# Performance work log

Hardware: AMD Instinct MI355X
Metric: run time of the kernel (lower is better)

The kernel has to match this reference:

```python
import jax, jax.numpy as jnp
import numpy as np

# RT-DETR matcher hyperparameters (from config)
ALPHA, GAMMA = 0.25, 2.0
C_CLASS, C_BBOX, C_GIOU = 2.0, 5.0, 2.0
B, Q, C, T = 32, 300, 80, 100  # batch, queries, classes, targets-per-image


def _center_to_corners(b):
    cx, cy, w, h = jnp.split(b, 4, axis=-1)
    return jnp.concatenate([cx - 0.5 * w, cy - 0.5 * h, cx + 0.5 * w, cy + 0.5 * h], axis=-1)


def _generalized_box_iou(boxes1, boxes2):
    # boxes1 [N,4], boxes2 [M,4] in corner format -> [N,M] GIoU
    area1 = (boxes1[:, 2] - boxes1[:, 0]) * (boxes1[:, 3] - boxes1[:, 1])
    area2 = (boxes2[:, 2] - boxes2[:, 0]) * (boxes2[:, 3] - boxes2[:, 1])
    lt = jnp.maximum(boxes1[:, None, :2], boxes2[None, :, :2])
    rb = jnp.minimum(boxes1[:, None, 2:], boxes2[None, :, 2:])
    wh = jnp.clip(rb - lt, 0.0)
    inter = wh[..., 0] * wh[..., 1]
    union = area1[:, None] + area2[None, :] - inter
    iou = inter / union
    lt_e = jnp.minimum(boxes1[:, None, :2], boxes2[None, :, :2])
    rb_e = jnp.maximum(boxes1[:, None, 2:], boxes2[None, :, 2:])
    wh_e = jnp.clip(rb_e - lt_e, 0.0)
    enclose = wh_e[..., 0] * wh_e[..., 1]
    return iou - (enclose - union) / enclose


def setup_inputs() -> dict:
    key = jax.random.key(0)
    k1, k2, k3, k4 = jax.random.split(key, 4)
    logits = jax.random.normal(k1, (B, Q, C), dtype=jnp.float32)
    pred_boxes = jax.random.uniform(k2, (B, Q, 4), dtype=jnp.float32)
    target_labels = jax.random.randint(k3, (B * T,), 0, C)
    target_boxes = jax.random.uniform(k4, (B * T, 4), dtype=jnp.float32)
    return {"logits": logits, "pred_boxes": pred_boxes,
            "target_labels": target_labels, "target_boxes": target_boxes}


def reference(logits, pred_boxes, target_labels, target_boxes):
    batch_size, num_queries, num_classes = logits.shape
    out_bbox = pred_boxes.reshape(-1, 4)                      # [B*Q, 4]
    # focal-style class cost (use_focal_loss=True)
    out_prob = jax.nn.sigmoid(logits.reshape(-1, num_classes))  # [B*Q, C]
    out_prob = out_prob[:, target_labels]                       # [B*Q, B*T]
    neg_cost = (1 - ALPHA) * out_prob ** GAMMA * -jnp.log(1 - out_prob + 1e-8)
    pos_cost = ALPHA * (1 - out_prob) ** GAMMA * -jnp.log(out_prob + 1e-8)
    class_cost = pos_cost - neg_cost
    # pairwise L1 cost on cxcywh boxes
    bbox_cost = jnp.sum(jnp.abs(out_bbox[:, None, :] - target_boxes[None, :, :]), axis=-1)
    # pairwise GIoU cost on corner boxes
    giou_cost = -_generalized_box_iou(_center_to_corners(out_bbox), _center_to_corners(target_boxes))
    cost_matrix = C_BBOX * bbox_cost + C_CLASS * class_cost + C_GIOU * giou_cost
    return cost_matrix.reshape(batch_size, num_queries, -1)    # [B, Q, B*T]
```

## Files before the change

### kernel.cpp

```cpp
#include <hip/hip_runtime.h>


constexpr int BB = 32, QQ = 300, CN = 80, TT = 100;
constexpr int NQ = BB * QQ;
constexpr int NT = BB * TT;
constexpr int JG = NT / 4;
constexpr int RCHUNK = 32;
constexpr int STRIPES = (JG + 255) / 256;
constexpr int CCN = RCHUNK * CN;

typedef float vfloat4 __attribute__((ext_vector_type(4)));

__global__ __launch_bounds__(256, 4) void fused_kernel(
    const float*  __restrict__ logits,
    const float4* __restrict__ pred_boxes,
    const int*    __restrict__ labels,
    const float4* __restrict__ target_boxes,
    float4*       __restrict__ out)
{
  const int tid  = threadIdx.x;
  const int jg   = blockIdx.x * 256 + tid;
  const int row0 = blockIdx.y * RCHUNK;

  __shared__ float  s_cc[CCN];
  __shared__ float4 s_pred[RCHUNK];

  const float* lgbase = logits + (size_t)row0 * CN;
#pragma unroll
  for (int i = 0; i < CCN / 256; ++i) {
    const int e = i * 256 + tid;
    float x = lgbase[e];
    float p = 1.0f / (1.0f + __expf(-x));
    float omp = 1.0f - p;
    float neg = 0.75f * p * p * (-__logf(omp + 1e-8f));
    float pos = 0.25f * omp * omp * (-__logf(p + 1e-8f));
    s_cc[e] = 2.0f * (pos - neg) + 2.0f;
  }
  if (tid < RCHUNK) s_pred[tid] = pred_boxes[row0 + tid];
  __syncthreads();
  if (jg >= JG) return;

  float tcx[4], tcy[4], tw[4], th[4];
  float tx0[4], ty0[4], tx1[4], ty1[4], ta[4];
  const float* ccbase[4];
#pragma unroll
  for (int k = 0; k < 4; ++k) {
    float4 t = target_boxes[jg * 4 + k];
    tcx[k] = t.x; tcy[k] = t.y; tw[k] = t.z; th[k] = t.w;
    tx0[k] = t.x - 0.5f * t.z;  ty0[k] = t.y - 0.5f * t.w;
    tx1[k] = t.x + 0.5f * t.z;  ty1[k] = t.y + 0.5f * t.w;
    ta[k]  = t.z * t.w;
    ccbase[k] = s_cc + labels[jg * 4 + k];
  }

  vfloat4* outp = reinterpret_cast<vfloat4*>(out + (size_t)row0 * JG + jg);

  for (int rb = 0; rb < RCHUNK; rb += 4) {
#pragma unroll
    for (int ri = 0; ri < 4; ++ri) {
      const int r = rb + ri;
      float4 p = s_pred[r];
      float px0 = p.x - 0.5f * p.z, py0 = p.y - 0.5f * p.w;
      float px1 = p.x + 0.5f * p.z, py1 = p.y + 0.5f * p.w;
      float pa  = p.z * p.w;

      float res[4];
#pragma unroll
      for (int k = 0; k < 4; ++k) {
        float l1 = fabsf(p.x - tcx[k]) + fabsf(p.y - tcy[k]) +
                   fabsf(p.z - tw[k])  + fabsf(p.w - th[k]);
        float ltx = fmaxf(px0, tx0[k]), lty = fmaxf(py0, ty0[k]);
        float rbx = fminf(px1, tx1[k]), rby = fminf(py1, ty1[k]);
        float iw = fmaxf(rbx - ltx, 0.0f), ih = fmaxf(rby - lty, 0.0f);
        float inter = iw * ih;
        float uni = pa + ta[k] - inter;
        float ex0 = fminf(px0, tx0[k]), ey0 = fminf(py0, ty0[k]);
        float ex1 = fmaxf(px1, tx1[k]), ey1 = fmaxf(py1, ty1[k]);
        float enc = (ex1 - ex0) * (ey1 - ey0);
        float iou = inter * __builtin_amdgcn_rcpf(uni);
        float une = uni   * __builtin_amdgcn_rcpf(enc);
        float cls = ccbase[k][r * CN];
        float acc = fmaf(5.0f, l1, cls);
        acc       = fmaf(-2.0f, iou, acc);
        res[k]    = fmaf(-2.0f, une, acc);
      }
      vfloat4 v = { res[0], res[1], res[2], res[3] };
      __builtin_nontemporal_store(v, &outp[(size_t)r * JG]);
    }
  }
}

extern "C" void kernel_launch(void* const* d_in, const int* in_sizes, int n_in,
                              void* d_out, int out_size, void* d_ws, size_t ws_size,
                              hipStream_t stream) {
  const float*  logits = (const float*)d_in[0];
  const float4* pred   = (const float4*)d_in[1];
  const int*    labels = (const int*)d_in[2];
  const float4* tboxes = (const float4*)d_in[3];
  float4* out = (float4*)d_out;

  dim3 grid(STRIPES, NQ / RCHUNK);
  fused_kernel<<<grid, 256, 0, stream>>>(logits, pred, labels, tboxes, out);
}
```

Baseline: 155.4 us.

## Transpose class-cost table in LDS and merge GIoU reciprocals into one

The shared class-cost table is stored transposed (class-major, padded stride 36). Each thread can then fetch four consecutive rows' costs for a label with one 128-bit LDS read instead of four scalar gathers. The GIoU term iou + union/enclose is rewritten over a common denominator, so it needs one reciprocal instead of two. The combined fraction may lose a little precision or overflow differently for extreme boxes, and the transposed stores during the table build may hit more LDS bank conflicts.

```diff
diff --git a/kernel.cpp b/kernel.cpp
--- a/kernel.cpp
+++ b/kernel.cpp
@@ -8,6 +8,7 @@
 constexpr int RCHUNK = 32;
 constexpr int STRIPES = (JG + 255) / 256;
 constexpr int CCN = RCHUNK * CN;
+constexpr int CS = 36;
 
 typedef float vfloat4 __attribute__((ext_vector_type(4)));
 
@@ -22,19 +23,20 @@
   const int jg   = blockIdx.x * 256 + tid;
   const int row0 = blockIdx.y * RCHUNK;
 
-  __shared__ float  s_cc[CCN];
+  __shared__ float  s_ccT[CN * CS];
   __shared__ float4 s_pred[RCHUNK];
 
   const float* lgbase = logits + (size_t)row0 * CN;
 #pragma unroll
   for (int i = 0; i < CCN / 256; ++i) {
     const int e = i * 256 + tid;
+    const int r = e / CN, c = e - r * CN;
     float x = lgbase[e];
     float p = 1.0f / (1.0f + __expf(-x));
     float omp = 1.0f - p;
     float neg = 0.75f * p * p * (-__logf(omp + 1e-8f));
     float pos = 0.25f * omp * omp * (-__logf(p + 1e-8f));
-    s_cc[e] = 2.0f * (pos - neg) + 2.0f;
+    s_ccT[c * CS + r] = 2.0f * (pos - neg) + 2.0f;
   }
   if (tid < RCHUNK) s_pred[tid] = pred_boxes[row0 + tid];
   __syncthreads();
@@ -42,7 +44,7 @@
 
   float tcx[4], tcy[4], tw[4], th[4];
   float tx0[4], ty0[4], tx1[4], ty1[4], ta[4];
-  const float* ccbase[4];
+  const float* ccT[4];
 #pragma unroll
   for (int k = 0; k < 4; ++k) {
     float4 t = target_boxes[jg * 4 + k];
@@ -50,16 +52,20 @@
     tx0[k] = t.x - 0.5f * t.z;  ty0[k] = t.y - 0.5f * t.w;
     tx1[k] = t.x + 0.5f * t.z;  ty1[k] = t.y + 0.5f * t.w;
     ta[k]  = t.z * t.w;
-    ccbase[k] = s_cc + labels[jg * 4 + k];
+    ccT[k] = s_ccT + labels[jg * 4 + k] * CS;
   }
 
   vfloat4* outp = reinterpret_cast<vfloat4*>(out + (size_t)row0 * JG + jg);
 
   for (int rb = 0; rb < RCHUNK; rb += 4) {
+    vfloat4 cls4[4];
+#pragma unroll
+    for (int k = 0; k < 4; ++k)
+      cls4[k] = *reinterpret_cast<const vfloat4*>(ccT[k] + rb);
+
 #pragma unroll
     for (int ri = 0; ri < 4; ++ri) {
-      const int r = rb + ri;
-      float4 p = s_pred[r];
+      float4 p = s_pred[rb + ri];
       float px0 = p.x - 0.5f * p.z, py0 = p.y - 0.5f * p.w;
       float px1 = p.x + 0.5f * p.z, py1 = p.y + 0.5f * p.w;
       float pa  = p.z * p.w;
@@ -77,15 +83,14 @@
         float ex0 = fminf(px0, tx0[k]), ey0 = fminf(py0, ty0[k]);
         float ex1 = fmaxf(px1, tx1[k]), ey1 = fmaxf(py1, ty1[k]);
         float enc = (ex1 - ex0) * (ey1 - ey0);
-        float iou = inter * __builtin_amdgcn_rcpf(uni);
-        float une = uni   * __builtin_amdgcn_rcpf(enc);
-        float cls = ccbase[k][r * CN];
-        float acc = fmaf(5.0f, l1, cls);
-        acc       = fmaf(-2.0f, iou, acc);
-        res[k]    = fmaf(-2.0f, une, acc);
+        float num = fmaf(uni, uni, inter * enc);
+        float den = uni * enc;
+        float ratio = num * __builtin_amdgcn_rcpf(den);
+        float acc = fmaf(5.0f, l1, cls4[k][ri]);
+        res[k]    = fmaf(-2.0f, ratio, acc);
       }
       vfloat4 v = { res[0], res[1], res[2], res[3] };
-      __builtin_nontemporal_store(v, &outp[(size_t)r * JG]);
+      __builtin_nontemporal_store(v, &outp[(size_t)(rb + ri) * JG]);
     }
   }
 }
```

Result: no change. 154.2 us (-0.7%).
